# Performance work log

Measured on AMD Instinct MI355X. Metric: run time of the kernel, lower is better.

## Reference

```python
import jax, jax.numpy as jnp
import numpy as np

D_MODEL = 1024
NHEAD = 16
D_K = D_MODEL // NHEAD


def setup_inputs() -> dict:
    key = jax.random.key(0)
    ks = jax.random.split(key, 11)
    B, S = 2, 2048
    scale = 1.0 / np.sqrt(D_MODEL)
    inp = {
        "q": jax.random.normal(ks[0], (B, S, D_MODEL), jnp.float32),
        "k": jax.random.normal(ks[1], (B, S, D_MODEL), jnp.float32),
        "v": jax.random.normal(ks[2], (B, S, D_MODEL), jnp.float32),
        "Wq": jax.random.normal(ks[3], (D_MODEL, D_MODEL), jnp.float32) * scale,
        "bq": jnp.zeros((D_MODEL,), jnp.float32),
        "Wk": jax.random.normal(ks[4], (D_MODEL, D_MODEL), jnp.float32) * scale,
        "bk": jnp.zeros((D_MODEL,), jnp.float32),
        "Wv": jax.random.normal(ks[5], (D_MODEL, D_MODEL), jnp.float32) * scale,
        "bv": jnp.zeros((D_MODEL,), jnp.float32),
        "Wo": jax.random.normal(ks[6], (D_MODEL, D_MODEL), jnp.float32) * scale,
        "bo": jnp.zeros((D_MODEL,), jnp.float32),
    }
    return inp


def reference(q, k, v, Wq, bq, Wk, bk, Wv, bv, Wo, bo):
    B, S, _ = q.shape
    # Linear projections (torch Linear: x @ W.T + b), split into heads
    def proj(x, W, b):
        y = jnp.einsum('bsd,ed->bse', x, W) + b
        return y.reshape(B, -1, NHEAD, D_K).transpose(0, 2, 1, 3)  # [B,H,S,Dk]

    qh = proj(q, Wq, bq)
    kh = proj(k, Wk, bk)
    vh = proj(v, Wv, bv)

    scores = jnp.einsum('bhqd,bhkd->bhqk', qh, kh) / jnp.sqrt(
        jnp.asarray(D_K, qh.dtype))
    attn = jax.nn.softmax(scores, axis=-1)  # dropout is identity in eval
    out = jnp.einsum('bhqk,bhkd->bhqd', attn, vh)
    out = out.transpose(0, 2, 1, 3).reshape(B, S, D_MODEL)
    return jnp.einsum('bsd,ed->bse', out, Wo) + bo
```

## Files before the change

kernel.cpp:

```cpp
#include <hip/hip_runtime.h>
#include <stdint.h>
#include <stddef.h>

#define D_MODEL 1024
#define NHEAD   16
#define DK      64
#define BB      2
#define SS      2048
#define NTOK    (BB*SS)

#define SCALE_Q 0.18033688011f

typedef short  short8 __attribute__((ext_vector_type(8)));
typedef __bf16 bf16x8 __attribute__((ext_vector_type(8)));
typedef float  f32x4  __attribute__((ext_vector_type(4)));

__device__ __forceinline__ unsigned short f2bf(float x){
  unsigned int u = __builtin_bit_cast(unsigned int, x);
  u += 0x7fffu + ((u >> 16) & 1u);
  return (unsigned short)(u >> 16);
}

__device__ __forceinline__ unsigned int pack_bf2(float x, float y){
  unsigned int a = __builtin_bit_cast(unsigned int, x) + 0x8000u;
  unsigned int b = __builtin_bit_cast(unsigned int, y) + 0x8000u;
  return __builtin_amdgcn_perm(b, a, 0x07060302u);
}

__device__ __forceinline__ float fast_exp2(float x){
#if __has_builtin(__builtin_amdgcn_exp2f)
  return __builtin_amdgcn_exp2f(x);
#else
  return exp2f(x);
#endif
}

__device__ __forceinline__ f32x4 mfma16(bf16x8 a, bf16x8 b, f32x4 c){
  return __builtin_amdgcn_mfma_f32_16x16x32_bf16(a, b, c, 0, 0, 0);
}

__device__ __forceinline__ void async16(const void* g, void* lds){
  __builtin_amdgcn_global_load_lds(
      (const __attribute__((address_space(1))) unsigned int*)g,
      (__attribute__((address_space(3))) unsigned int*)lds,
      16, 0, 0);
}

__global__ __launch_bounds__(256) void cast_bf16_all(
    const float* __restrict__ q,  const float* __restrict__ k,  const float* __restrict__ v,
    const float* __restrict__ wq, const float* __restrict__ wk, const float* __restrict__ wv,
    const float* __restrict__ wo,
    unsigned short* __restrict__ qb,  unsigned short* __restrict__ kb,  unsigned short* __restrict__ vb,
    unsigned short* __restrict__ wqb, unsigned short* __restrict__ wkb, unsigned short* __restrict__ wvb,
    unsigned short* __restrict__ wob)
{
  const float* src; unsigned short* dst; int n;
  switch (blockIdx.y){
    case 0: src = q;  dst = qb;  n = NTOK*D_MODEL;    break;
    case 1: src = k;  dst = kb;  n = NTOK*D_MODEL;    break;
    case 2: src = v;  dst = vb;  n = NTOK*D_MODEL;    break;
    case 3: src = wq; dst = wqb; n = D_MODEL*D_MODEL; break;
    case 4: src = wk; dst = wkb; n = D_MODEL*D_MODEL; break;
    case 5: src = wv; dst = wvb; n = D_MODEL*D_MODEL; break;
    default: src = wo; dst = wob; n = D_MODEL*D_MODEL; break;
  }
  int i = (blockIdx.x * 256 + threadIdx.x) * 8;
  if (i >= n) return;
  float4 a = *(const float4*)(src + i);
  float4 b = *(const float4*)(src + i + 4);
  short8 o;
  o[0] = (short)f2bf(a.x); o[1] = (short)f2bf(a.y);
  o[2] = (short)f2bf(a.z); o[3] = (short)f2bf(a.w);
  o[4] = (short)f2bf(b.x); o[5] = (short)f2bf(b.y);
  o[6] = (short)f2bf(b.z); o[7] = (short)f2bf(b.w);
  *(short8*)(dst + i) = o;
}

__global__ __launch_bounds__(256) void qkv_gemm(
    const unsigned short* __restrict__ qb, const unsigned short* __restrict__ kb,
    const unsigned short* __restrict__ vb,
    const unsigned short* __restrict__ wqb, const unsigned short* __restrict__ wkb,
    const unsigned short* __restrict__ wvb,
    const float* __restrict__ bq, const float* __restrict__ bk, const float* __restrict__ bv,
    unsigned short* __restrict__ Qh, unsigned short* __restrict__ Kh, unsigned short* __restrict__ Vt)
{
  __shared__ __align__(16) unsigned short As[128*64];
  __shared__ __align__(16) unsigned short Bs[128*64];
  const int id = blockIdx.x, z = id >> 8, r = id & 255;
  const unsigned short *A, *Bt; const float* bias; unsigned short* C;
  int bm, bn, N, brow; float scale;
  if (z == 0){ A = qb;  Bt = wqb; bias = bq; C = Qh; bm = (r>>3)*128; bn = (r&7)*128; N = 1024; brow = 0; scale = SCALE_Q; }
  else if (z == 1){ A = kb;  Bt = wkb; bias = bk; C = Kh; bm = (r>>3)*128; bn = (r&7)*128; N = 1024; brow = 0; scale = 1.0f; }
  else            { A = wvb; Bt = vb;  bias = bv; C = Vt; bm = (r&7)*128; bn = (r>>3)*128; N = 4096; brow = 1; scale = 1.0f; }
  const int K = 1024;
  const int tid  = threadIdx.x, lane = tid & 63, w = tid >> 6;
  const int quad = lane >> 4,   l16  = lane & 15;
  const int wm = w >> 1, wn = w & 1;
  const int sw = l16 & 7;
  f32x4 acc[4][4] = {};
  for (int kb_ = 0; kb_ < 16; ++kb_){
    const int k0 = kb_ << 6;
    __syncthreads();
    #pragma unroll
    for (int c = 0; c < 4; ++c){
      int chunk = (w*4 + c)*64 + lane;
      int row = chunk >> 3, c8 = chunk & 7;
      int cs = (c8 ^ (row & 7)) << 3;
      async16(A  + (size_t)(bm + row)*K + k0 + cs, (char*)As + (w*4 + c)*1024);
      async16(Bt + (size_t)(bn + row)*K + k0 + cs, (char*)Bs + (w*4 + c)*1024);
    }
    __syncthreads();
    bf16x8 af[4][2], bf[4][2];
    #pragma unroll
    for (int mt = 0; mt < 4; ++mt)
      #pragma unroll
      for (int ks = 0; ks < 2; ++ks){
        int off = (((ks*4 + quad) ^ sw) << 3);
        af[mt][ks] = *(const bf16x8*)&As[(wm*64 + mt*16 + l16)*64 + off];
        bf[mt][ks] = *(const bf16x8*)&Bs[(wn*64 + mt*16 + l16)*64 + off];
      }
    #pragma unroll
    for (int ks = 0; ks < 2; ++ks)
      #pragma unroll
      for (int mt = 0; mt < 4; ++mt)
        #pragma unroll
        for (int nt = 0; nt < 4; ++nt)
          acc[mt][nt] = mfma16(af[mt][ks], bf[nt][ks], acc[mt][nt]);
  }
  const int m0 = bm + wm*64, n0 = bn + wn*64;
  #pragma unroll
  for (int mt = 0; mt < 4; ++mt){
    #pragma unroll
    for (int nt = 0; nt < 4; ++nt){
      int col = n0 + nt*16 + l16;
      float bc = brow ? 0.0f : bias[col];
      #pragma unroll
      for (int rr = 0; rr < 4; ++rr){
        int row = m0 + mt*16 + quad*4 + rr;
        float val = (acc[mt][nt][rr] + (brow ? bias[row] : bc)) * scale;
        C[(size_t)row*N + col] = f2bf(val);
      }
    }
  }
}

__global__ __launch_bounds__(256) void gemm_out(
    const unsigned short* __restrict__ A, const unsigned short* __restrict__ Bt,
    const float* __restrict__ bias, float* __restrict__ C)
{
  __shared__ __align__(16) unsigned short As[64*64];
  __shared__ __align__(16) unsigned short Bs[128*64];
  const int K = 1024, N = 1024;
  const int tid  = threadIdx.x, lane = tid & 63, w = tid >> 6;
  const int quad = lane >> 4,   l16  = lane & 15;
  const int bm = blockIdx.y * 64, bn = blockIdx.x * 128;
  const int sw = l16 & 7;
  f32x4 acc[4][2] = {};
  for (int kb_ = 0; kb_ < 16; ++kb_){
    const int k0 = kb_ << 6;
    __syncthreads();
    #pragma unroll
    for (int c = 0; c < 2; ++c){
      int chunk = (w*2 + c)*64 + lane;
      int row = chunk >> 3, c8 = chunk & 7;
      async16(A + (size_t)(bm + row)*K + k0 + ((c8 ^ (row & 7)) << 3),
              (char*)As + (w*2 + c)*1024);
    }
    #pragma unroll
    for (int c = 0; c < 4; ++c){
      int chunk = (w*4 + c)*64 + lane;
      int row = chunk >> 3, c8 = chunk & 7;
      async16(Bt + (size_t)(bn + row)*K + k0 + ((c8 ^ (row & 7)) << 3),
              (char*)Bs + (w*4 + c)*1024);
    }
    __syncthreads();
    bf16x8 af[4][2], bf[2][2];
    #pragma unroll
    for (int mt = 0; mt < 4; ++mt)
      #pragma unroll
      for (int ks = 0; ks < 2; ++ks)
        af[mt][ks] = *(const bf16x8*)&As[(mt*16 + l16)*64 + (((ks*4 + quad) ^ sw) << 3)];
    #pragma unroll
    for (int nt = 0; nt < 2; ++nt)
      #pragma unroll
      for (int ks = 0; ks < 2; ++ks)
        bf[nt][ks] = *(const bf16x8*)&Bs[(w*32 + nt*16 + l16)*64 + (((ks*4 + quad) ^ sw) << 3)];
    #pragma unroll
    for (int ks = 0; ks < 2; ++ks)
      #pragma unroll
      for (int mt = 0; mt < 4; ++mt)
        #pragma unroll
        for (int nt = 0; nt < 2; ++nt)
          acc[mt][nt] = mfma16(af[mt][ks], bf[nt][ks], acc[mt][nt]);
  }
  #pragma unroll
  for (int mt = 0; mt < 4; ++mt){
    #pragma unroll
    for (int nt = 0; nt < 2; ++nt){
      int col = bn + w*32 + nt*16 + l16;
      float bc = bias[col];
      #pragma unroll
      for (int rr = 0; rr < 4; ++rr){
        int row = bm + mt*16 + quad*4 + rr;
        C[(size_t)row*N + col] = acc[mt][nt][rr] + bc;
      }
    }
  }
}

__global__ __launch_bounds__(256) void attn(
    const unsigned short* __restrict__ Qh, const unsigned short* __restrict__ Kh,
    const unsigned short* __restrict__ Vt, unsigned short* __restrict__ ctx)
{
  __shared__ __align__(16) unsigned short Kbuf[64*64];
  __shared__ __align__(16) unsigned short Vbuf[64*64];
  __shared__ __align__(16) unsigned short QP[128*64];

  const int tid  = threadIdx.x, lane = tid & 63, w = tid >> 6;
  const int quad = lane >> 4,   l16  = lane & 15;
  const int b = blockIdx.y >> 4, h = blockIdx.y & 15;
  const int q0 = blockIdx.x * 128;
  const int sw = l16 & 7;

  #pragma unroll
  for (int c = 0; c < 4; ++c){
    int s = (w*4 + c)*64 + lane;
    int row = s >> 3, c8 = s & 7;
    async16(Qh + (size_t)(b*SS + q0 + row)*D_MODEL + h*DK + ((c8 ^ (row & 7)) << 3),
            (char*)QP + (w*4 + c)*1024);
  }
  __syncthreads();
  bf16x8 bq[2][2];
  #pragma unroll
  for (int qg = 0; qg < 2; ++qg)
    #pragma unroll
    for (int ks = 0; ks < 2; ++ks)
      bq[qg][ks] = *(const bf16x8*)&QP[(w*32 + qg*16 + l16)*64 + (((ks*4 + quad) ^ sw) << 3)];

  const unsigned short* Kp = Kh + (size_t)(b*SS)*D_MODEL + h*DK;
  const unsigned short* Vp = Vt + (size_t)(h*DK)*NTOK + b*SS;
  const unsigned short* ksrc[2];
  const unsigned short* vsrc[2];
  #pragma unroll
  for (int c = 0; c < 2; ++c){
    int s = (w*2 + c)*64 + lane;
    int row = s >> 3, c8 = s & 7;
    int cs = (c8 ^ (row & 7)) << 3;
    ksrc[c] = Kp + (size_t)row*D_MODEL + cs;
    vsrc[c] = Vp + (size_t)row*NTOK  + cs;
  }

  f32x4 acc[2][4] = {};
  float l_i[2] = {0.0f, 0.0f};

  for (int kv0 = 0; kv0 < SS; kv0 += 64){
    __syncthreads();
    #pragma unroll
    for (int c = 0; c < 2; ++c){
      async16(ksrc[c], (char*)Kbuf + (w*2 + c)*1024);
      async16(vsrc[c], (char*)Vbuf + (w*2 + c)*1024);
      ksrc[c] += 64*D_MODEL;
      vsrc[c] += 64;
    }
    __syncthreads();

    bf16x8 kf[4][2];
    #pragma unroll
    for (int mt = 0; mt < 4; ++mt)
      #pragma unroll
      for (int ks = 0; ks < 2; ++ks)
        kf[mt][ks] = *(const bf16x8*)&Kbuf[(mt*16 + l16)*64 + (((ks*4 + quad) ^ sw) << 3)];

    #pragma unroll
    for (int qg = 0; qg < 2; ++qg){
      f32x4 s[4] = {};
      #pragma unroll
      for (int mt = 0; mt < 4; ++mt)
        #pragma unroll
        for (int ks = 0; ks < 2; ++ks)
          s[mt] = mfma16(kf[mt][ks], bq[qg][ks], s[mt]);
      float ls = 0.0f;
      #pragma unroll
      for (int mt = 0; mt < 4; ++mt)
        #pragma unroll
        for (int rr = 0; rr < 4; ++rr){
          float p = fast_exp2(s[mt][rr]); s[mt][rr] = p; ls += p;
        }
      l_i[qg] += ls;
      const int pr = (w*32 + qg*16 + l16)*64;
      #pragma unroll
      for (int mt = 0; mt < 4; ++mt){
        int c8  = mt*2 + (quad >> 1);
        int off = ((c8 ^ sw) << 3) + (quad & 1)*4;
        uint2 p;
        p.x = pack_bf2(s[mt][0], s[mt][1]);
        p.y = pack_bf2(s[mt][2], s[mt][3]);
        *(uint2*)&QP[pr + off] = p;
      }
    }
    asm volatile("" ::: "memory");

    bf16x8 vf[4][2];
    #pragma unroll
    for (int nt = 0; nt < 4; ++nt)
      #pragma unroll
      for (int ks = 0; ks < 2; ++ks)
        vf[nt][ks] = *(const bf16x8*)&Vbuf[(nt*16 + l16)*64 + (((ks*4 + quad) ^ sw) << 3)];
    #pragma unroll
    for (int qg = 0; qg < 2; ++qg){
      bf16x8 bp[2];
      #pragma unroll
      for (int ks = 0; ks < 2; ++ks)
        bp[ks] = *(const bf16x8*)&QP[(w*32 + qg*16 + l16)*64 + (((ks*4 + quad) ^ sw) << 3)];
      #pragma unroll
      for (int nt = 0; nt < 4; ++nt)
        #pragma unroll
        for (int ks = 0; ks < 2; ++ks)
          acc[qg][nt] = mfma16(vf[nt][ks], bp[ks], acc[qg][nt]);
    }
  }

  float inv[2];
  #pragma unroll
  for (int qg = 0; qg < 2; ++qg){
    float t = l_i[qg];
    t += __shfl_xor(t, 16);
    t += __shfl_xor(t, 32);
    inv[qg] = 1.0f / t;
  }
  #pragma unroll
  for (int qg = 0; qg < 2; ++qg){
    int pr = (w*32 + qg*16 + l16)*64;
    #pragma unroll
    for (int nt = 0; nt < 4; ++nt){
      int c8  = nt*2 + (quad >> 1);
      int off = ((c8 ^ sw) << 3) + (quad & 1)*4;
      uint2 p;
      p.x = pack_bf2(acc[qg][nt][0]*inv[qg], acc[qg][nt][1]*inv[qg]);
      p.y = pack_bf2(acc[qg][nt][2]*inv[qg], acc[qg][nt][3]*inv[qg]);
      *(uint2*)&QP[pr + off] = p;
    }
  }
  asm volatile("s_waitcnt lgkmcnt(0)" ::: "memory");
  {
    int r  = w*32 + (lane >> 1);
    int j0 = (lane & 1)*4;
    unsigned short* dst = ctx + (size_t)(b*SS + q0 + r)*D_MODEL + h*DK;
    #pragma unroll
    for (int i = 0; i < 4; ++i){
      int j = j0 + i;
      uint4 d = *(const uint4*)&QP[r*64 + ((j ^ (r & 7)) << 3)];
      *(uint4*)(dst + j*8) = d;
    }
  }
}

extern "C" void kernel_launch(void* const* d_in, const int* in_sizes, int n_in,
                              void* d_out, int out_size, void* d_ws, size_t ws_size,
                              hipStream_t stream) {
  const float* q  = (const float*)d_in[0];
  const float* k  = (const float*)d_in[1];
  const float* v  = (const float*)d_in[2];
  const float* Wq = (const float*)d_in[3];
  const float* bq = (const float*)d_in[4];
  const float* Wk = (const float*)d_in[5];
  const float* bk = (const float*)d_in[6];
  const float* Wv = (const float*)d_in[7];
  const float* bv = (const float*)d_in[8];
  const float* Wo = (const float*)d_in[9];
  const float* bo = (const float*)d_in[10];

  char* ws = (char*)d_ws;
  const size_t TOKB = (size_t)NTOK * D_MODEL * 2;
  const size_t WB   = (size_t)D_MODEL * D_MODEL * 2;
  unsigned short* qb  = (unsigned short*)ws;             ws += TOKB;
  unsigned short* kb  = (unsigned short*)ws;             ws += TOKB;
  unsigned short* vb  = (unsigned short*)ws;             ws += TOKB;
  unsigned short* wqb = (unsigned short*)ws;             ws += WB;
  unsigned short* wkb = (unsigned short*)ws;             ws += WB;
  unsigned short* wvb = (unsigned short*)ws;             ws += WB;
  unsigned short* wob = (unsigned short*)ws;             ws += WB;
  unsigned short* Qh  = (unsigned short*)ws;             ws += TOKB;
  unsigned short* Kh  = (unsigned short*)ws;             ws += TOKB;
  unsigned short* Vt  = (unsigned short*)ws;             ws += TOKB;
  unsigned short* ctx = (unsigned short*)ws;             ws += TOKB;

  cast_bf16_all<<<dim3(2048, 7), 256, 0, stream>>>(q, k, v, Wq, Wk, Wv, Wo,
                                                   qb, kb, vb, wqb, wkb, wvb, wob);
  qkv_gemm<<<dim3(768), 256, 0, stream>>>(qb, kb, vb, wqb, wkb, wvb,
                                          bq, bk, bv, Qh, Kh, Vt);
  attn<<<dim3(SS/128, BB*NHEAD), 256, 0, stream>>>(Qh, Kh, Vt, ctx);
  gemm_out<<<dim3(8, 64), 256, 0, stream>>>(ctx, wob, bo, (float*)d_out);
}
```

Measured before the change: 235.2 us.

## Load 128-key K/V tiles per barrier pair and interleave two query groups

The attention loop now stages 128 keys of K and V into shared memory per iteration instead of 64, which halves the number of barrier pairs and global-to-LDS rounds. Each 128-key tile is processed in two 64-key halves. V uses a 128-wide row layout with a 16-way XOR swizzle. The MFMA and exp work for the two query groups is interleaved to expose more independent instructions, and an explicit LDS wait is placed before the P reads. The cost is double the LDS for K/V, which may reduce occupancy, and more live registers.

```diff
diff --git a/kernel.cpp b/kernel.cpp
--- a/kernel.cpp
+++ b/kernel.cpp
@@ -212,8 +212,8 @@
     const unsigned short* __restrict__ Qh, const unsigned short* __restrict__ Kh,
     const unsigned short* __restrict__ Vt, unsigned short* __restrict__ ctx)
 {
-  __shared__ __align__(16) unsigned short Kbuf[64*64];
-  __shared__ __align__(16) unsigned short Vbuf[64*64];
+  __shared__ __align__(16) unsigned short Kbuf[128*64];
+  __shared__ __align__(16) unsigned short Vbuf[64*128];
   __shared__ __align__(16) unsigned short QP[128*64];
 
   const int tid  = threadIdx.x, lane = tid & 63, w = tid >> 6;
@@ -230,93 +230,99 @@
             (char*)QP + (w*4 + c)*1024);
   }
   __syncthreads();
-  bf16x8 bq[2][2];
-  #pragma unroll
-  for (int qg = 0; qg < 2; ++qg)
-    #pragma unroll
-    for (int ks = 0; ks < 2; ++ks)
-      bq[qg][ks] = *(const bf16x8*)&QP[(w*32 + qg*16 + l16)*64 + (((ks*4 + quad) ^ sw) << 3)];
+  bf16x8 bq0[2], bq1[2];
+  #pragma unroll
+  for (int ks = 0; ks < 2; ++ks){
+    bq0[ks] = *(const bf16x8*)&QP[(w*32 +      l16)*64 + (((ks*4 + quad) ^ sw) << 3)];
+    bq1[ks] = *(const bf16x8*)&QP[(w*32 + 16 + l16)*64 + (((ks*4 + quad) ^ sw) << 3)];
+  }
 
   const unsigned short* Kp = Kh + (size_t)(b*SS)*D_MODEL + h*DK;
   const unsigned short* Vp = Vt + (size_t)(h*DK)*NTOK + b*SS;
-  const unsigned short* ksrc[2];
-  const unsigned short* vsrc[2];
-  #pragma unroll
-  for (int c = 0; c < 2; ++c){
-    int s = (w*2 + c)*64 + lane;
-    int row = s >> 3, c8 = s & 7;
-    int cs = (c8 ^ (row & 7)) << 3;
-    ksrc[c] = Kp + (size_t)row*D_MODEL + cs;
-    vsrc[c] = Vp + (size_t)row*NTOK  + cs;
+  const unsigned short* ksrc[4];
+  const unsigned short* vsrc[4];
+  #pragma unroll
+  for (int c = 0; c < 4; ++c){
+    int s = (w*4 + c)*64 + lane;
+    int kr = s >> 3, kc = s & 7;
+    ksrc[c] = Kp + (size_t)kr*D_MODEL + ((kc ^ (kr & 7)) << 3);
+    int vr = s >> 4, vc = s & 15;
+    vsrc[c] = Vp + (size_t)vr*NTOK + ((vc ^ (vr & 15)) << 3);
   }
 
   f32x4 acc[2][4] = {};
   float l_i[2] = {0.0f, 0.0f};
 
-  for (int kv0 = 0; kv0 < SS; kv0 += 64){
-    __syncthreads();
-    #pragma unroll
-    for (int c = 0; c < 2; ++c){
-      async16(ksrc[c], (char*)Kbuf + (w*2 + c)*1024);
-      async16(vsrc[c], (char*)Vbuf + (w*2 + c)*1024);
-      ksrc[c] += 64*D_MODEL;
-      vsrc[c] += 64;
-    }
-    __syncthreads();
-
-    bf16x8 kf[4][2];
-    #pragma unroll
-    for (int mt = 0; mt < 4; ++mt)
-      #pragma unroll
-      for (int ks = 0; ks < 2; ++ks)
-        kf[mt][ks] = *(const bf16x8*)&Kbuf[(mt*16 + l16)*64 + (((ks*4 + quad) ^ sw) << 3)];
-
-    #pragma unroll
-    for (int qg = 0; qg < 2; ++qg){
-      f32x4 s[4] = {};
+  for (int it = 0; it < 16; ++it){
+    __syncthreads();
+    #pragma unroll
+    for (int c = 0; c < 4; ++c){
+      async16(ksrc[c], (char*)Kbuf + (w*4 + c)*1024);
+      async16(vsrc[c], (char*)Vbuf + (w*4 + c)*1024);
+      ksrc[c] += 128*D_MODEL;
+      vsrc[c] += 128;
+    }
+    __syncthreads();
+
+    #pragma unroll
+    for (int half = 0; half < 2; ++half){
+      bf16x8 kf[4][2];
       #pragma unroll
       for (int mt = 0; mt < 4; ++mt)
         #pragma unroll
         for (int ks = 0; ks < 2; ++ks)
-          s[mt] = mfma16(kf[mt][ks], bq[qg][ks], s[mt]);
-      float ls = 0.0f;
+          kf[mt][ks] = *(const bf16x8*)&Kbuf[(half*64 + mt*16 + l16)*64 + (((ks*4 + quad) ^ sw) << 3)];
+
+      f32x4 s0[4] = {}, s1[4] = {};
+      #pragma unroll
+      for (int mt = 0; mt < 4; ++mt)
+        #pragma unroll
+        for (int ks = 0; ks < 2; ++ks){
+          s0[mt] = mfma16(kf[mt][ks], bq0[ks], s0[mt]);
+          s1[mt] = mfma16(kf[mt][ks], bq1[ks], s1[mt]);
+        }
+
+      float ls0 = 0.0f, ls1 = 0.0f;
       #pragma unroll
       for (int mt = 0; mt < 4; ++mt)
         #pragma unroll
         for (int rr = 0; rr < 4; ++rr){
-          float p = fast_exp2(s[mt][rr]); s[mt][rr] = p; ls += p;
+          float p0 = fast_exp2(s0[mt][rr]); s0[mt][rr] = p0; ls0 += p0;
+          float p1 = fast_exp2(s1[mt][rr]); s1[mt][rr] = p1; ls1 += p1;
         }
-      l_i[qg] += ls;
-      const int pr = (w*32 + qg*16 + l16)*64;
+      l_i[0] += ls0; l_i[1] += ls1;
+      const int pr0 = (w*32 +      l16)*64;
+      const int pr1 = (w*32 + 16 + l16)*64;
       #pragma unroll
       for (int mt = 0; mt < 4; ++mt){
         int c8  = mt*2 + (quad >> 1);
         int off = ((c8 ^ sw) << 3) + (quad & 1)*4;
         uint2 p;
-        p.x = pack_bf2(s[mt][0], s[mt][1]);
-        p.y = pack_bf2(s[mt][2], s[mt][3]);
-        *(uint2*)&QP[pr + off] = p;
-      }
-    }
-    asm volatile("" ::: "memory");
-
-    bf16x8 vf[4][2];
-    #pragma unroll
-    for (int nt = 0; nt < 4; ++nt)
-      #pragma unroll
-      for (int ks = 0; ks < 2; ++ks)
-        vf[nt][ks] = *(const bf16x8*)&Vbuf[(nt*16 + l16)*64 + (((ks*4 + quad) ^ sw) << 3)];
-    #pragma unroll
-    for (int qg = 0; qg < 2; ++qg){
-      bf16x8 bp[2];
-      #pragma unroll
-      for (int ks = 0; ks < 2; ++ks)
-        bp[ks] = *(const bf16x8*)&QP[(w*32 + qg*16 + l16)*64 + (((ks*4 + quad) ^ sw) << 3)];
-      #pragma unroll
-      for (int nt = 0; nt < 4; ++nt)
-        #pragma unroll
-        for (int ks = 0; ks < 2; ++ks)
-          acc[qg][nt] = mfma16(vf[nt][ks], bp[ks], acc[qg][nt]);
+        p.x = pack_bf2(s0[mt][0], s0[mt][1]);
+        p.y = pack_bf2(s0[mt][2], s0[mt][3]);
+        *(uint2*)&QP[pr0 + off] = p;
+        p.x = pack_bf2(s1[mt][0], s1[mt][1]);
+        p.y = pack_bf2(s1[mt][2], s1[mt][3]);
+        *(uint2*)&QP[pr1 + off] = p;
+      }
+      asm volatile("s_waitcnt lgkmcnt(0)" ::: "memory");
+      bf16x8 bp0[2], bp1[2];
+      #pragma unroll
+      for (int ks = 0; ks < 2; ++ks){
+        bp0[ks] = *(const bf16x8*)&QP[pr0 + (((ks*4 + quad) ^ sw) << 3)];
+        bp1[ks] = *(const bf16x8*)&QP[pr1 + (((ks*4 + quad) ^ sw) << 3)];
+      }
+
+      #pragma unroll
+      for (int nt = 0; nt < 4; ++nt){
+        bf16x8 vf0, vf1;
+        vf0 = *(const bf16x8*)&Vbuf[(nt*16 + l16)*128 + (((half*8 + quad)     ^ l16) << 3)];
+        vf1 = *(const bf16x8*)&Vbuf[(nt*16 + l16)*128 + (((half*8 + 4 + quad) ^ l16) << 3)];
+        acc[0][nt] = mfma16(vf0, bp0[0], acc[0][nt]);
+        acc[1][nt] = mfma16(vf0, bp1[0], acc[1][nt]);
+        acc[0][nt] = mfma16(vf1, bp0[1], acc[0][nt]);
+        acc[1][nt] = mfma16(vf1, bp1[1], acc[1][nt]);
+      }
     }
   }
 
```

Measured after the change: 235.9 us. About the same (+0.3%).
